# Optimization experiments

Hardware: AMD Instinct MI355X
Metric: run time of the kernel (lower is better)

## Reference

```python
import jax, jax.numpy as jnp
import numpy as np

B, D, H, W, C = 2, 128, 128, 128, 8
GD = GH = GW = 96


def setup_inputs() -> dict:
    key = jax.random.key(0)
    k1, k2 = jax.random.split(key)
    inputs = jax.random.normal(k1, (B, D, H, W, C), dtype=jnp.float32)
    # sample_coords uniform over the valid voxel range [0, size-1] per spatial dim
    sizes = jnp.array([D - 1, H - 1, W - 1], dtype=jnp.float32)
    sample_coords = jax.random.uniform(k2, (B, GD, GH, GW, 3), dtype=jnp.float32) * sizes
    return {"inputs": inputs, "sample_coords": sample_coords}


def reference(inputs, sample_coords):
    # Trilinear resampling with REPLICATE boundary (clamp), matching
    # ResamplerLayer.resample_linear + boundary_replicate.
    input_size = inputs.shape[1:-1]                       # (D, H, W)
    rank = len(input_size)                                # 3
    floor_c = jnp.floor(sample_coords)                    # [B, gd, gh, gw, 3]
    w = sample_coords - floor_c                           # fractional weights
    wc = 1.0 - w
    i0 = floor_c.astype(jnp.int32)
    c0 = [jnp.clip(i0[..., d], 0, input_size[d] - 1) for d in range(rank)]
    c1 = [jnp.clip(i0[..., d] + 1, 0, input_size[d] - 1) for d in range(rank)]

    bsz = sample_coords.shape[0]
    batch_idx = jnp.arange(bsz).reshape((bsz,) + (1,) * (sample_coords.ndim - 2))

    # Sum over the 2^rank corners; identical math to the recursive
    # pyramid_combination in the original (fixed small unrolled loop).
    out = jnp.zeros(sample_coords.shape[:-1] + (inputs.shape[-1],), inputs.dtype)
    for code in range(2 ** rank):
        bits = [(code >> (rank - 1 - d)) & 1 for d in range(rank)]
        idx = [c1[d] if bits[d] else c0[d] for d in range(rank)]
        samp = inputs[batch_idx, idx[0], idx[1], idx[2]]  # [B, gd, gh, gw, C]
        wt = jnp.ones(sample_coords.shape[:-1], inputs.dtype)
        for d in range(rank):
            wt = wt * (w[..., d] if bits[d] else wc[..., d])
        out = out + samp * wt[..., None]
    return out
```

## Files before the change

kernel.cpp:

```cpp
#include <hip/hip_runtime.h>
#include <stdint.h>


constexpr int B  = 2;
constexpr int D  = 128;
constexpr int H  = 128;
constexpr int W  = 128;
constexpr int C  = 8;
constexpr int GD = 96;
constexpr int GH = 96;
constexpr int GW = 96;
constexpr long long PTS_PER_B = (long long)GD * GH * GW;
constexpr long long NPTS      = (long long)B * PTS_PER_B;
constexpr int NPTS_I = (int)NPTS;

constexpr int TPZ = 16, TPY = 16, TPX = 16;
constexpr int NT_PER_B = TPZ * TPY * TPX;
constexpr int NT = B * NT_PER_B;

constexpr int RZ = 9, RY = 9, RX = 9;
constexpr int RVOX = RZ * RY * RX;

constexpr int TPB_BIN = 1024;
constexpr int PPT     = 8;
constexpr int NB_BIN  = NPTS_I / (TPB_BIN * PPT);
static_assert(NB_BIN * TPB_BIN * PPT == NPTS_I, "exact tiling");
constexpr int BPT = NT / TPB_BIN;

__device__ __forceinline__ int clampi(int v, int lo, int hi) {
    return min(max(v, lo), hi);
}

__device__ __forceinline__ int tile_of(int b, float zc, float yc, float xc) {
    int z0 = clampi((int)floorf(zc), 0, D - 1);
    int y0 = clampi((int)floorf(yc), 0, H - 1);
    int x0 = clampi((int)floorf(xc), 0, W - 1);
    return (b << 12) | ((z0 >> 3) << 8) | ((y0 >> 3) << 4) | (x0 >> 3);
}

__device__ __forceinline__ uint32_t bf16_rne(float f) {
    uint32_t u = __float_as_uint(f);
    u += 0x7FFFu + ((u >> 16) & 1u);
    return u >> 16;
}
__device__ __forceinline__ uint32_t pack_bf16(float lo, float hi) {
    return bf16_rne(lo) | (bf16_rne(hi) << 16);
}

__global__ __launch_bounds__(TPB_BIN)
void k_hist(const float* __restrict__ coords, uint16_t* __restrict__ blockHist)
{
    __shared__ uint32_t h[NT];
    const int t = threadIdx.x;
#pragma unroll
    for (int j = 0; j < BPT; ++j) h[t + j * TPB_BIN] = 0u;
    __syncthreads();

    const int base = blockIdx.x * (TPB_BIN * PPT);
#pragma unroll
    for (int k = 0; k < PPT; ++k) {
        const int i = base + k * TPB_BIN + t;
        const float zc = coords[3 * i + 0];
        const float yc = coords[3 * i + 1];
        const float xc = coords[3 * i + 2];
        const int b = (i >= (int)PTS_PER_B) ? 1 : 0;
        atomicAdd(&h[tile_of(b, zc, yc, xc)], 1u);
    }
    __syncthreads();
#pragma unroll
    for (int j = 0; j < BPT; ++j) {
        const int c = t + j * TPB_BIN;
        blockHist[blockIdx.x * NT + c] = (uint16_t)h[c];
    }
}

__global__ __launch_bounds__(128)
void k_scan_cols(uint16_t* __restrict__ blockHist, uint32_t* __restrict__ bucketTot)
{
    const int c = blockIdx.x * 128 + threadIdx.x;
    uint32_t acc = 0u;
#pragma unroll 8
    for (int r = 0; r < NB_BIN; ++r) {
        const int o = r * NT + c;
        const uint32_t v = blockHist[o];
        blockHist[o] = (uint16_t)acc;
        acc += v;
    }
    bucketTot[c] = acc;
}

__global__ __launch_bounds__(TPB_BIN)
void k_scan_base(const uint32_t* __restrict__ bucketTot, uint32_t* __restrict__ bucketBase)
{
    __shared__ uint32_t ss[TPB_BIN];
    const int t = threadIdx.x;

    uint32_t l[BPT];
    uint32_t ls = 0u;
#pragma unroll
    for (int j = 0; j < BPT; ++j) {
        l[j] = bucketTot[t * BPT + j];
        ls += l[j];
    }
    ss[t] = ls;
    __syncthreads();
    for (int off = 1; off < TPB_BIN; off <<= 1) {
        const uint32_t v = (t >= off) ? ss[t - off] : 0u;
        __syncthreads();
        ss[t] += v;
        __syncthreads();
    }
    uint32_t basev = ss[t] - ls;
#pragma unroll
    for (int j = 0; j < BPT; ++j) {
        bucketBase[t * BPT + j] = basev;
        basev += l[j];
    }
    if (t == TPB_BIN - 1) bucketBase[NT] = (uint32_t)NPTS_I;
}

__global__ __launch_bounds__(TPB_BIN)
void k_scatter(const float* __restrict__ coords,
               const uint16_t* __restrict__ blockHist,
               const uint32_t* __restrict__ bucketBase,
               float4* __restrict__ records)
{
    __shared__ uint32_t cur[NT];
    const int t = threadIdx.x;
#pragma unroll
    for (int j = 0; j < BPT; ++j) {
        const int c = t + j * TPB_BIN;
        cur[c] = (uint32_t)blockHist[blockIdx.x * NT + c] + bucketBase[c];
    }
    __syncthreads();

    const int base = blockIdx.x * (TPB_BIN * PPT);
#pragma unroll
    for (int k = 0; k < PPT; ++k) {
        const int i = base + k * TPB_BIN + t;
        const float zc = coords[3 * i + 0];
        const float yc = coords[3 * i + 1];
        const float xc = coords[3 * i + 2];
        const int b = (i >= (int)PTS_PER_B) ? 1 : 0;
        const int tk = tile_of(b, zc, yc, xc);
        const uint32_t slot = atomicAdd(&cur[tk], 1u);
        records[slot] = make_float4(zc, yc, xc, __uint_as_float((uint32_t)i));
    }
}

__global__ __launch_bounds__(128)
void k_sample_tiled(const float* __restrict__ inp,
                    const float4* __restrict__ records,
                    const uint32_t* __restrict__ bucketBase,
                    float* __restrict__ out)
{
    __shared__ uint4 tile[RVOX];
    const int t = threadIdx.x;

    const int g = blockIdx.x;
    const int c = (g & 7) * (NT >> 3) + (g >> 3);

    const int tx = c & 15;
    const int ty = (c >> 4) & 15;
    const int tz = (c >> 8) & 15;
    const int b  = c >> 12;
    const int z0r = tz << 3, y0r = ty << 3, x0r = tx << 3;

    for (int v = t; v < RVOX; v += 128) {
        const int lz = v / (RY * RX);
        const int rr = v - lz * (RY * RX);
        const int ly = rr / RX;
        const int lx = rr - ly * RX;
        const int gz = min(z0r + lz, D - 1);
        const int gy = min(y0r + ly, H - 1);
        const int gx = min(x0r + lx, W - 1);
        const int a = ((((b << 7) | gz) << 7 | gy) << 7 | gx) * C;
        const float4 v0 = *reinterpret_cast<const float4*>(inp + a);
        const float4 v1 = *reinterpret_cast<const float4*>(inp + a + 4);
        uint4 pk;
        pk.x = pack_bf16(v0.x, v0.y);
        pk.y = pack_bf16(v0.z, v0.w);
        pk.z = pack_bf16(v1.x, v1.y);
        pk.w = pack_bf16(v1.z, v1.w);
        tile[v] = pk;
    }
    __syncthreads();

    const uint32_t start = bucketBase[c];
    const uint32_t end   = bucketBase[c + 1];

    for (uint32_t i = start + t; i < end; i += 128) {
        const float4 rec = records[i];
        const float zc = rec.x, yc = rec.y, xc = rec.z;
        const int idx = (int)__float_as_uint(rec.w);

        const float fz = floorf(zc);
        const float fy = floorf(yc);
        const float fx = floorf(xc);
        const float wz1 = zc - fz, wz0 = 1.0f - wz1;
        const float wy1 = yc - fy, wy0 = 1.0f - wy1;
        const float wx1 = xc - fx, wx0 = 1.0f - wx1;

        const int lz = clampi((int)fz, 0, D - 1) - z0r;
        const int ly = clampi((int)fy, 0, H - 1) - y0r;
        const int lx = clampi((int)fx, 0, W - 1) - x0r;
        const int vi = (lz * RY + ly) * RX + lx;

        float a0 = 0.f, a1 = 0.f, a2 = 0.f, a3 = 0.f;
        float a4 = 0.f, a5 = 0.f, a6 = 0.f, a7 = 0.f;
        const float wzs[2] = {wz0, wz1};
        const float wys[2] = {wy0, wy1};
        const float wxs[2] = {wx0, wx1};

#pragma unroll
        for (int iz = 0; iz < 2; ++iz) {
#pragma unroll
            for (int iy = 0; iy < 2; ++iy) {
#pragma unroll
                for (int ix = 0; ix < 2; ++ix) {
                    const float wt = wzs[iz] * wys[iy] * wxs[ix];
                    const int cv = vi + (iz * RY + iy) * RX + ix;
                    const uint4 rv = tile[cv];
                    a0 += wt * __uint_as_float(rv.x << 16);
                    a1 += wt * __uint_as_float(rv.x & 0xFFFF0000u);
                    a2 += wt * __uint_as_float(rv.y << 16);
                    a3 += wt * __uint_as_float(rv.y & 0xFFFF0000u);
                    a4 += wt * __uint_as_float(rv.z << 16);
                    a5 += wt * __uint_as_float(rv.z & 0xFFFF0000u);
                    a6 += wt * __uint_as_float(rv.w << 16);
                    a7 += wt * __uint_as_float(rv.w & 0xFFFF0000u);
                }
            }
        }

        float* o = out + (long long)idx * C;
        *reinterpret_cast<float4*>(o)     = make_float4(a0, a1, a2, a3);
        *reinterpret_cast<float4*>(o + 4) = make_float4(a4, a5, a6, a7);
    }
}

__global__ __launch_bounds__(256)
void resample_direct(const float* __restrict__ inp,
                     const float* __restrict__ coords,
                     float* __restrict__ out)
{
    const long long i = (long long)blockIdx.x * blockDim.x + threadIdx.x;
    if (i >= NPTS) return;
    const int b = (i >= PTS_PER_B) ? 1 : 0;
    const float zc = coords[3 * i + 0];
    const float yc = coords[3 * i + 1];
    const float xc = coords[3 * i + 2];
    const float fz = floorf(zc), fy = floorf(yc), fx = floorf(xc);
    const float wz1 = zc - fz, wz0 = 1.0f - wz1;
    const float wy1 = yc - fy, wy0 = 1.0f - wy1;
    const float wx1 = xc - fx, wx0 = 1.0f - wx1;
    const int z0 = clampi((int)fz, 0, D - 1);
    const int y0 = clampi((int)fy, 0, H - 1);
    const int x0 = clampi((int)fx, 0, W - 1);
    const int z1 = min(z0 + 1, D - 1);
    const int y1 = min(y0 + 1, H - 1);
    const int x1 = min(x0 + 1, W - 1);
    float4 acc_lo = make_float4(0.f, 0.f, 0.f, 0.f);
    float4 acc_hi = make_float4(0.f, 0.f, 0.f, 0.f);
    const int   zs[2]  = {z0, z1};
    const int   ys[2]  = {y0, y1};
    const int   xs[2]  = {x0, x1};
    const float wzs[2] = {wz0, wz1};
    const float wys[2] = {wy0, wy1};
    const float wxs[2] = {wx0, wx1};
#pragma unroll
    for (int iz = 0; iz < 2; ++iz)
#pragma unroll
        for (int iy = 0; iy < 2; ++iy)
#pragma unroll
            for (int ix = 0; ix < 2; ++ix) {
                const float wt = wzs[iz] * wys[iy] * wxs[ix];
                const int base = ((((b << 7) | zs[iz]) << 7 | ys[iy]) << 7 | xs[ix]) * C;
                const float4 v0 = *reinterpret_cast<const float4*>(inp + base);
                const float4 v1 = *reinterpret_cast<const float4*>(inp + base + 4);
                acc_lo.x += wt * v0.x;  acc_lo.y += wt * v0.y;
                acc_lo.z += wt * v0.z;  acc_lo.w += wt * v0.w;
                acc_hi.x += wt * v1.x;  acc_hi.y += wt * v1.y;
                acc_hi.z += wt * v1.z;  acc_hi.w += wt * v1.w;
            }
    float* o = out + i * C;
    *reinterpret_cast<float4*>(o)     = acc_lo;
    *reinterpret_cast<float4*>(o + 4) = acc_hi;
}

extern "C" void kernel_launch(void* const* d_in, const int* in_sizes, int n_in,
                              void* d_out, int out_size, void* d_ws, size_t ws_size,
                              hipStream_t stream)
{
    const float* inp    = (const float*)d_in[0];
    const float* coords = (const float*)d_in[1];
    float* out          = (float*)d_out;

    const size_t rec_bytes  = (size_t)NPTS_I * sizeof(float4);
    const size_t hist_bytes = (size_t)NB_BIN * NT * sizeof(uint16_t);
    const size_t base_bytes = (size_t)(NT + 1) * sizeof(uint32_t);
    const size_t tot_bytes  = (size_t)NT * sizeof(uint32_t);
    const size_t needed     = rec_bytes + hist_bytes + base_bytes + tot_bytes;

    if (ws_size < needed) {
        const int nblk = (NPTS_I + 255) / 256;
        resample_direct<<<nblk, 256, 0, stream>>>(inp, coords, out);
        return;
    }

    float4*   records    = (float4*)d_ws;
    uint16_t* blockHist  = (uint16_t*)((char*)d_ws + rec_bytes);
    uint32_t* bucketBase = (uint32_t*)((char*)d_ws + rec_bytes + hist_bytes);
    uint32_t* bucketTot  = (uint32_t*)((char*)d_ws + rec_bytes + hist_bytes + base_bytes);

    k_hist        <<<NB_BIN,   TPB_BIN, 0, stream>>>(coords, blockHist);
    k_scan_cols   <<<NT / 128, 128,     0, stream>>>(blockHist, bucketTot);
    k_scan_base   <<<1,        TPB_BIN, 0, stream>>>(bucketTot, bucketBase);
    k_scatter     <<<NB_BIN,   TPB_BIN, 0, stream>>>(coords, blockHist, bucketBase, records);
    k_sample_tiled<<<NT,       128,     0, stream>>>(inp, records, bucketBase, out);
}
```

Before: 94.59 us.

## Compress sort records to 64-bit and double-buffer tile loads across buckets

```diff
diff --git a/kernel.cpp b/kernel.cpp
--- a/kernel.cpp
+++ b/kernel.cpp
@@ -27,6 +27,9 @@
 static_assert(NB_BIN * TPB_BIN * PPT == NPTS_I, "exact tiling");
 constexpr int BPT = NT / TPB_BIN;
 
+constexpr int BUCKETS_PER_BLOCK = 4;
+constexpr int NBLK4 = NT / BUCKETS_PER_BLOCK;
+
 __device__ __forceinline__ int clampi(int v, int lo, int hi) {
     return min(max(v, lo), hi);
 }
@@ -36,6 +39,23 @@
     int y0 = clampi((int)floorf(yc), 0, H - 1);
     int x0 = clampi((int)floorf(xc), 0, W - 1);
     return (b << 12) | ((z0 >> 3) << 8) | ((y0 >> 3) << 4) | (x0 >> 3);
+}
+
+__device__ __forceinline__ unsigned long long
+pack_rec(int i, float zc, float yc, float xc, int b, int& tk)
+{
+    const int z0 = clampi((int)floorf(zc), 0, D - 1);
+    const int y0 = clampi((int)floorf(yc), 0, H - 1);
+    const int x0 = clampi((int)floorf(xc), 0, W - 1);
+    const int tz = z0 >> 3, ty = y0 >> 3, tx = x0 >> 3;
+    tk = (b << 12) | (tz << 8) | (ty << 4) | tx;
+    const int qz = clampi((int)((zc - (float)(tz << 3)) * 1024.0f + 0.5f), 0, 8191);
+    const int qy = clampi((int)((yc - (float)(ty << 3)) * 1024.0f + 0.5f), 0, 8191);
+    const int qx = clampi((int)((xc - (float)(tx << 3)) * 1024.0f + 0.5f), 0, 8191);
+    return (unsigned long long)(uint32_t)i
+         | ((unsigned long long)qx << 21)
+         | ((unsigned long long)qy << 34)
+         | ((unsigned long long)qz << 47);
 }
 
 __device__ __forceinline__ uint32_t bf16_rne(float f) {
@@ -123,7 +143,7 @@
 void k_scatter(const float* __restrict__ coords,
                const uint16_t* __restrict__ blockHist,
                const uint32_t* __restrict__ bucketBase,
-               float4* __restrict__ records)
+               unsigned long long* __restrict__ records)
 {
     __shared__ uint32_t cur[NT];
     const int t = threadIdx.x;
@@ -142,100 +162,134 @@
         const float yc = coords[3 * i + 1];
         const float xc = coords[3 * i + 2];
         const int b = (i >= (int)PTS_PER_B) ? 1 : 0;
-        const int tk = tile_of(b, zc, yc, xc);
+        int tk;
+        const unsigned long long r = pack_rec(i, zc, yc, xc, b, tk);
         const uint32_t slot = atomicAdd(&cur[tk], 1u);
-        records[slot] = make_float4(zc, yc, xc, __uint_as_float((uint32_t)i));
-    }
-}
-
-__global__ __launch_bounds__(128)
+        records[slot] = r;
+    }
+}
+
+__device__ __forceinline__ void
+process_rec(unsigned long long r, const uint4* __restrict__ tb,
+            float* __restrict__ out)
+{
+    const int idx = (int)(r & 0x1FFFFFull);
+    const int qx  = (int)((r >> 21) & 0x1FFFull);
+    const int qy  = (int)((r >> 34) & 0x1FFFull);
+    const int qz  = (int)((r >> 47) & 0x1FFFull);
+    const int lx = qx >> 10, ly = qy >> 10, lz = qz >> 10;
+    const float wx1 = (float)(qx & 1023) * (1.0f / 1024.0f), wx0 = 1.0f - wx1;
+    const float wy1 = (float)(qy & 1023) * (1.0f / 1024.0f), wy0 = 1.0f - wy1;
+    const float wz1 = (float)(qz & 1023) * (1.0f / 1024.0f), wz0 = 1.0f - wz1;
+
+    const int vi = (lz * RY + ly) * RX + lx;
+
+    float a0 = 0.f, a1 = 0.f, a2 = 0.f, a3 = 0.f;
+    float a4 = 0.f, a5 = 0.f, a6 = 0.f, a7 = 0.f;
+    const float wzs[2] = {wz0, wz1};
+    const float wys[2] = {wy0, wy1};
+    const float wxs[2] = {wx0, wx1};
+
+#pragma unroll
+    for (int iz = 0; iz < 2; ++iz) {
+#pragma unroll
+        for (int iy = 0; iy < 2; ++iy) {
+#pragma unroll
+            for (int ix = 0; ix < 2; ++ix) {
+                const float wt = wzs[iz] * wys[iy] * wxs[ix];
+                const int cv = vi + (iz * RY + iy) * RX + ix;
+                const uint4 rv = tb[cv];
+                a0 += wt * __uint_as_float(rv.x << 16);
+                a1 += wt * __uint_as_float(rv.x & 0xFFFF0000u);
+                a2 += wt * __uint_as_float(rv.y << 16);
+                a3 += wt * __uint_as_float(rv.y & 0xFFFF0000u);
+                a4 += wt * __uint_as_float(rv.z << 16);
+                a5 += wt * __uint_as_float(rv.z & 0xFFFF0000u);
+                a6 += wt * __uint_as_float(rv.w << 16);
+                a7 += wt * __uint_as_float(rv.w & 0xFFFF0000u);
+            }
+        }
+    }
+
+    float* o = out + (long long)idx * C;
+    *reinterpret_cast<float4*>(o)     = make_float4(a0, a1, a2, a3);
+    *reinterpret_cast<float4*>(o + 4) = make_float4(a4, a5, a6, a7);
+}
+
+__global__ __launch_bounds__(256)
 void k_sample_tiled(const float* __restrict__ inp,
-                    const float4* __restrict__ records,
+                    const unsigned long long* __restrict__ records,
                     const uint32_t* __restrict__ bucketBase,
                     float* __restrict__ out)
 {
-    __shared__ uint4 tile[RVOX];
+    __shared__ uint4 tile[2][RVOX];
     const int t = threadIdx.x;
 
-    const int g = blockIdx.x;
-    const int c = (g & 7) * (NT >> 3) + (g >> 3);
-
-    const int tx = c & 15;
-    const int ty = (c >> 4) & 15;
-    const int tz = (c >> 8) & 15;
-    const int b  = c >> 12;
-    const int z0r = tz << 3, y0r = ty << 3, x0r = tx << 3;
-
-    for (int v = t; v < RVOX; v += 128) {
-        const int lz = v / (RY * RX);
-        const int rr = v - lz * (RY * RX);
-        const int ly = rr / RX;
-        const int lx = rr - ly * RX;
-        const int gz = min(z0r + lz, D - 1);
-        const int gy = min(y0r + ly, H - 1);
-        const int gx = min(x0r + lx, W - 1);
-        const int a = ((((b << 7) | gz) << 7 | gy) << 7 | gx) * C;
-        const float4 v0 = *reinterpret_cast<const float4*>(inp + a);
-        const float4 v1 = *reinterpret_cast<const float4*>(inp + a + 4);
-        uint4 pk;
-        pk.x = pack_bf16(v0.x, v0.y);
-        pk.y = pack_bf16(v0.z, v0.w);
-        pk.z = pack_bf16(v1.x, v1.y);
-        pk.w = pack_bf16(v1.z, v1.w);
-        tile[v] = pk;
-    }
-    __syncthreads();
-
-    const uint32_t start = bucketBase[c];
-    const uint32_t end   = bucketBase[c + 1];
-
-    for (uint32_t i = start + t; i < end; i += 128) {
-        const float4 rec = records[i];
-        const float zc = rec.x, yc = rec.y, xc = rec.z;
-        const int idx = (int)__float_as_uint(rec.w);
-
-        const float fz = floorf(zc);
-        const float fy = floorf(yc);
-        const float fx = floorf(xc);
-        const float wz1 = zc - fz, wz0 = 1.0f - wz1;
-        const float wy1 = yc - fy, wy0 = 1.0f - wy1;
-        const float wx1 = xc - fx, wx0 = 1.0f - wx1;
-
-        const int lz = clampi((int)fz, 0, D - 1) - z0r;
-        const int ly = clampi((int)fy, 0, H - 1) - y0r;
-        const int lx = clampi((int)fx, 0, W - 1) - x0r;
-        const int vi = (lz * RY + ly) * RX + lx;
-
-        float a0 = 0.f, a1 = 0.f, a2 = 0.f, a3 = 0.f;
-        float a4 = 0.f, a5 = 0.f, a6 = 0.f, a7 = 0.f;
-        const float wzs[2] = {wz0, wz1};
-        const float wys[2] = {wy0, wy1};
-        const float wxs[2] = {wx0, wx1};
-
-#pragma unroll
-        for (int iz = 0; iz < 2; ++iz) {
-#pragma unroll
-            for (int iy = 0; iy < 2; ++iy) {
-#pragma unroll
-                for (int ix = 0; ix < 2; ++ix) {
-                    const float wt = wzs[iz] * wys[iy] * wxs[ix];
-                    const int cv = vi + (iz * RY + iy) * RX + ix;
-                    const uint4 rv = tile[cv];
-                    a0 += wt * __uint_as_float(rv.x << 16);
-                    a1 += wt * __uint_as_float(rv.x & 0xFFFF0000u);
-                    a2 += wt * __uint_as_float(rv.y << 16);
-                    a3 += wt * __uint_as_float(rv.y & 0xFFFF0000u);
-                    a4 += wt * __uint_as_float(rv.z << 16);
-                    a5 += wt * __uint_as_float(rv.z & 0xFFFF0000u);
-                    a6 += wt * __uint_as_float(rv.w << 16);
-                    a7 += wt * __uint_as_float(rv.w & 0xFFFF0000u);
-                }
+    const int gb = ((int)blockIdx.x & 7) * (NBLK4 >> 3) + ((int)blockIdx.x >> 3);
+    const int c0 = gb * BUCKETS_PER_BLOCK;
+
+    float4 pv0[3], pv1[3];
+    unsigned long long pr = 0ull;
+    bool pr_valid = false;
+
+    auto issue_voxels = [&](int c) {
+        const int tx = c & 15, ty = (c >> 4) & 15, tz = (c >> 8) & 15, b = c >> 12;
+        const int z0r = tz << 3, y0r = ty << 3, x0r = tx << 3;
+#pragma unroll
+        for (int j = 0; j < 3; ++j) {
+            const int v = t + j * 256;
+            if (v < RVOX) {
+                const int lz = v / (RY * RX);
+                const int rr = v - lz * (RY * RX);
+                const int ly = rr / RX;
+                const int lx = rr - ly * RX;
+                const int gz = min(z0r + lz, D - 1);
+                const int gy = min(y0r + ly, H - 1);
+                const int gx = min(x0r + lx, W - 1);
+                const int a = ((((b << 7) | gz) << 7 | gy) << 7 | gx) * C;
+                pv0[j] = *reinterpret_cast<const float4*>(inp + a);
+                pv1[j] = *reinterpret_cast<const float4*>(inp + a + 4);
             }
         }
-
-        float* o = out + (long long)idx * C;
-        *reinterpret_cast<float4*>(o)     = make_float4(a0, a1, a2, a3);
-        *reinterpret_cast<float4*>(o + 4) = make_float4(a4, a5, a6, a7);
+    };
+    auto issue_rec = [&](int c) {
+        const uint32_t s = bucketBase[c];
+        const uint32_t e = bucketBase[c + 1];
+        const uint32_t i = s + (uint32_t)t;
+        pr_valid = (i < e);
+        if (pr_valid) pr = records[i];
+    };
+
+    issue_voxels(c0);
+    issue_rec(c0);
+
+    for (int k = 0; k < BUCKETS_PER_BLOCK; ++k) {
+        const int c = c0 + k;
+        uint4* tb = tile[k & 1];
+
+#pragma unroll
+        for (int j = 0; j < 3; ++j) {
+            const int v = t + j * 256;
+            if (v < RVOX) {
+                uint4 pk;
+                pk.x = pack_bf16(pv0[j].x, pv0[j].y);
+                pk.y = pack_bf16(pv0[j].z, pv0[j].w);
+                pk.z = pack_bf16(pv1[j].x, pv1[j].y);
+                pk.w = pack_bf16(pv1[j].z, pv1[j].w);
+                tb[v] = pk;
+            }
+        }
+        const uint32_t s = bucketBase[c];
+        const uint32_t e = bucketBase[c + 1];
+        const unsigned long long r0 = pr;
+        const bool r0v = pr_valid;
+        __syncthreads();
+
+        if (k + 1 < BUCKETS_PER_BLOCK) { issue_voxels(c + 1); issue_rec(c + 1); }
+
+        if (r0v) process_rec(r0, tb, out);
+        for (uint32_t i = s + (uint32_t)t + 256u; i < e; i += 256u)
+            process_rec(records[i], tb, out);
     }
 }
 
@@ -296,7 +350,7 @@
     const float* coords = (const float*)d_in[1];
     float* out          = (float*)d_out;
 
-    const size_t rec_bytes  = (size_t)NPTS_I * sizeof(float4);
+    const size_t rec_bytes  = (size_t)NPTS_I * sizeof(unsigned long long);
     const size_t hist_bytes = (size_t)NB_BIN * NT * sizeof(uint16_t);
     const size_t base_bytes = (size_t)(NT + 1) * sizeof(uint32_t);
     const size_t tot_bytes  = (size_t)NT * sizeof(uint32_t);
@@ -308,7 +362,7 @@
         return;
     }
 
-    float4*   records    = (float4*)d_ws;
+    unsigned long long* records = (unsigned long long*)d_ws;
     uint16_t* blockHist  = (uint16_t*)((char*)d_ws + rec_bytes);
     uint32_t* bucketBase = (uint32_t*)((char*)d_ws + rec_bytes + hist_bytes);
     uint32_t* bucketTot  = (uint32_t*)((char*)d_ws + rec_bytes + hist_bytes + base_bytes);
@@ -317,5 +371,5 @@
     k_scan_cols   <<<NT / 128, 128,     0, stream>>>(blockHist, bucketTot);
     k_scan_base   <<<1,        TPB_BIN, 0, stream>>>(bucketTot, bucketBase);
     k_scatter     <<<NB_BIN,   TPB_BIN, 0, stream>>>(coords, blockHist, bucketBase, records);
-    k_sample_tiled<<<NT,       128,     0, stream>>>(inp, records, bucketBase, out);
-}
+    k_sample_tiled<<<NBLK4,    256,     0, stream>>>(inp, records, bucketBase, out);
+}
```

Result: no change. 95.66 us (+1.1%).
